# Optimization experiments

Measured on AMD Instinct MI355X. Metric: run time of the kernel, lower is better.

## Reference

```python
import jax, jax.numpy as jnp
import numpy as np

GAMMA = 1.0
NUM_CLASSES = 128


def setup_inputs() -> dict:
    key = jax.random.key(0)
    k1, k2, k3 = jax.random.split(key, 3)
    B, D, P = 8192, 512, 4096
    feature = jax.random.normal(k1, (B, D), dtype=jnp.float32)
    label = jax.random.randint(k2, (B,), 0, NUM_CLASSES)
    proto_features = jax.random.normal(k3, (P, D), dtype=jnp.float32)
    proto_labels = jnp.arange(P) % NUM_CLASSES  # every class has prototypes
    return {"feature": feature, "label": label,
            "proto_features": proto_features, "proto_labels": proto_labels}


def reference(feature, label, proto_features, proto_labels):
    # squared euclidean distances [B, P] via ||f||^2 + ||p||^2 - 2 f.p
    f_sq = jnp.sum(feature * feature, axis=-1, keepdims=True)          # [B,1]
    p_sq = jnp.sum(proto_features * proto_features, axis=-1)           # [P]
    d2 = f_sq + p_sq[None, :] - 2.0 * (feature @ proto_features.T)      # [B,P]
    d2 = jnp.maximum(d2, 0.0)
    logits = -GAMMA * d2                                                # [B,P]
    # denominator: sum over ALL prototypes; numerator: sum over own-class protos
    log_den = jax.scipy.special.logsumexp(logits, axis=-1)              # [B]
    same = proto_labels[None, :] == label[:, None]                      # [B,P]
    neg_inf = jnp.finfo(logits.dtype).min
    log_num = jax.scipy.special.logsumexp(
        jnp.where(same, logits, neg_inf), axis=-1)                      # [B]
    # loss = -log(num/den) per sample
    return log_den - log_num
```

## Files before the change

### kernel.cpp

```cpp
#include <hip/hip_runtime.h>
#include <hip/hip_bf16.h>

#define BN 8192
#define DK 512
#define PN 4096
#define GY 8
#define PPB 512
#define CH 32
#define NCH 16
#define STRIDE 520
#define SENT (-1.0e30f)
#define L2E 1.4426950408889634f
#define LN2 0.6931471805599453f

typedef __bf16 bf16x8 __attribute__((ext_vector_type(8)));
typedef __bf16 bf16x4 __attribute__((ext_vector_type(4)));
typedef float f32x4 __attribute__((ext_vector_type(4)));

__device__ __forceinline__ float ex2(float x) { return __builtin_amdgcn_exp2f(x); }

__device__ __forceinline__ void gl_lds16(const void* g, void* l) {
    __builtin_amdgcn_global_load_lds(
        (const __attribute__((address_space(1))) void*)g,
        (__attribute__((address_space(3))) void*)l, 16, 0, 0);
}

__global__ __launch_bounds__(256) void k_prep(const float* __restrict__ proto,
                                              __bf16* __restrict__ pB,
                                              float* __restrict__ p_sq) {
    int p  = blockIdx.x * 4 + (threadIdx.x >> 6);
    int ln = threadIdx.x & 63;
    const float* src = proto + (size_t)p * DK;
    float4 a = *(const float4*)(src + ln * 4);
    float4 b = *(const float4*)(src + 256 + ln * 4);
    float s = a.x * a.x + a.y * a.y + a.z * a.z + a.w * a.w
            + b.x * b.x + b.y * b.y + b.z * b.z + b.w * b.w;
#pragma unroll
    for (int m = 1; m < 64; m <<= 1) s += __shfl_xor(s, m, 64);
    int sidx = (p & 127) * 32 + (p >> 7);
    bf16x4 c0, c1;
    c0[0] = (__bf16)a.x; c0[1] = (__bf16)a.y; c0[2] = (__bf16)a.z; c0[3] = (__bf16)a.w;
    c1[0] = (__bf16)b.x; c1[1] = (__bf16)b.y; c1[2] = (__bf16)b.z; c1[3] = (__bf16)b.w;
    *(bf16x4*)(pB + (size_t)sidx * DK + ln * 4) = c0;
    *(bf16x4*)(pB + (size_t)sidx * DK + 256 + ln * 4) = c1;
    if (ln == 0) p_sq[sidx] = s * L2E;
}

__global__ __launch_bounds__(256, 2) void k_main(
        const float* __restrict__ feat,
        const __bf16* __restrict__ pB,
        const float* __restrict__ p_sq,
        const int* __restrict__ label,
        float4* __restrict__ part) {

    __shared__ __bf16 sM[2 * CH * STRIDE];
    __shared__ float  sPsq[PPB];

    const int t    = threadIdx.x;
    const int w    = t >> 6;
    const int l    = t & 63;
    const int ln   = l & 15;
    const int quad = l >> 4;
    const int bx   = blockIdx.x;
    const int gy   = blockIdx.y;
    const int rw   = bx * 128 + w * 32;
    const int p0   = gy * PPB;

    int lab[2][4];
#pragma unroll
    for (int mf = 0; mf < 2; ++mf)
#pragma unroll
        for (int r = 0; r < 4; ++r)
            lab[mf][r] = label[rw + mf * 16 + quad * 4 + r];

    {
        const __bf16* g = pB + (size_t)(p0 + w * 8) * DK + l * 8;
        __bf16* lp = sM + (w * 8) * STRIDE;
#pragma unroll
        for (int j = 0; j < 8; ++j)
            gl_lds16(g + j * DK, lp + j * STRIDE);
    }
    sPsq[t]       = p_sq[p0 + t];
    sPsq[t + 256] = p_sq[p0 + t + 256];

    __bf16* sA = sM + CH * STRIDE;
    bf16x8 afrag[2][16];
#pragma unroll 1
    for (int q = 0; q < 4; ++q) {
#pragma unroll 4
        for (int i = 0; i < 16; ++i) {
            int idx = t + 256 * i;
            int row = idx >> 7;
            int c4  = idx & 127;
            float4 v = *(const float4*)(feat + (size_t)(bx * 128 + q * 32 + row) * DK + c4 * 4);
            bf16x4 cv;
            cv[0] = (__bf16)v.x; cv[1] = (__bf16)v.y; cv[2] = (__bf16)v.z; cv[3] = (__bf16)v.w;
            *(bf16x4*)(sA + row * STRIDE + c4 * 4) = cv;
        }
        __syncthreads();
        if (w == q) {
#pragma unroll
            for (int mf = 0; mf < 2; ++mf)
#pragma unroll
                for (int ks = 0; ks < 16; ++ks)
                    afrag[mf][ks] = *(const bf16x8*)(sA + (mf * 16 + ln) * STRIDE + ks * 32 + quad * 8);
        }
        __syncthreads();
    }

    float Md[2][4], Sd[2][4], Mn[2][4], Sn[2][4];
#pragma unroll
    for (int mf = 0; mf < 2; ++mf)
#pragma unroll
        for (int r = 0; r < 4; ++r) {
            Md[mf][r] = SENT; Sd[mf][r] = 0.f;
            Mn[mf][r] = SENT; Sn[mf][r] = 0.f;
        }

#pragma unroll 1
    for (int nt = 0; nt < NCH; ++nt) {
        if (nt + 1 < NCH) {
            const __bf16* g = pB + (size_t)(p0 + (nt + 1) * CH + w * 8) * DK + l * 8;
            __bf16* lp = sM + (((nt + 1) & 1) * CH + w * 8) * STRIDE;
#pragma unroll
            for (int j = 0; j < 8; ++j)
                gl_lds16(g + j * DK, lp + j * STRIDE);
        }

        const __bf16* sB = sM + (nt & 1) * CH * STRIDE;

        f32x4 acc[2][2];
#pragma unroll
        for (int mf = 0; mf < 2; ++mf)
#pragma unroll
            for (int nf = 0; nf < 2; ++nf)
                acc[mf][nf] = (f32x4){0.f, 0.f, 0.f, 0.f};

#pragma unroll
        for (int ks = 0; ks < 16; ++ks) {
            bf16x8 b0 = *(const bf16x8*)(sB + ln * STRIDE + ks * 32 + quad * 8);
            bf16x8 b1 = *(const bf16x8*)(sB + (16 + ln) * STRIDE + ks * 32 + quad * 8);
            acc[0][0] = __builtin_amdgcn_mfma_f32_16x16x32_bf16(afrag[0][ks], b0, acc[0][0], 0, 0, 0);
            acc[0][1] = __builtin_amdgcn_mfma_f32_16x16x32_bf16(afrag[0][ks], b1, acc[0][1], 0, 0, 0);
            acc[1][0] = __builtin_amdgcn_mfma_f32_16x16x32_bf16(afrag[1][ks], b0, acc[1][0], 0, 0, 0);
            acc[1][1] = __builtin_amdgcn_mfma_f32_16x16x32_bf16(afrag[1][ks], b1, acc[1][1], 0, 0, 0);
        }

        float nps0 = -sPsq[nt * 32 + ln];
        float nps1 = -sPsq[nt * 32 + 16 + ln];
        const int cls = gy * 16 + nt;

        float z[2][2][4];
#pragma unroll
        for (int mf = 0; mf < 2; ++mf)
#pragma unroll
            for (int r = 0; r < 4; ++r) {
                z[mf][0][r] = fmaf(acc[mf][0][r], 2.0f * L2E, nps0);
                z[mf][1][r] = fmaf(acc[mf][1][r], 2.0f * L2E, nps1);
            }

#pragma unroll
        for (int mf = 0; mf < 2; ++mf)
#pragma unroll
            for (int r = 0; r < 4; ++r) {
                float z0 = z[mf][0][r], z1 = z[mf][1][r];
                float nm = fmaxf(Md[mf][r], fmaxf(z0, z1));
                float e  = ex2(z0 - nm) + ex2(z1 - nm);
                Sd[mf][r] = fmaf(Sd[mf][r], ex2(Md[mf][r] - nm), e);
                Md[mf][r] = nm;
            }

        int anyhit = 0;
#pragma unroll
        for (int mf = 0; mf < 2; ++mf)
#pragma unroll
            for (int r = 0; r < 4; ++r)
                anyhit |= (cls == lab[mf][r]);
        if (__any(anyhit)) {
#pragma unroll
            for (int mf = 0; mf < 2; ++mf)
#pragma unroll
                for (int r = 0; r < 4; ++r) {
                    bool hit = (cls == lab[mf][r]);
                    float z0 = z[mf][0][r], z1 = z[mf][1][r];
                    float nm = fmaxf(Mn[mf][r], fmaxf(z0, z1));
                    float e  = ex2(z0 - nm) + ex2(z1 - nm);
                    float sn = fmaf(Sn[mf][r], ex2(Mn[mf][r] - nm), e);
                    Sn[mf][r] = hit ? sn : Sn[mf][r];
                    Mn[mf][r] = hit ? nm : Mn[mf][r];
                }
        }
        __syncthreads();
    }

#pragma unroll
    for (int mf = 0; mf < 2; ++mf)
#pragma unroll
        for (int r = 0; r < 4; ++r) {
            float md = Md[mf][r], sd = Sd[mf][r];
            float mn = Mn[mf][r], sn = Sn[mf][r];
#pragma unroll
            for (int m = 1; m < 16; m <<= 1) {
                float omd = __shfl_xor(md, m, 64);
                float osd = __shfl_xor(sd, m, 64);
                float omn = __shfl_xor(mn, m, 64);
                float osn = __shfl_xor(sn, m, 64);
                float nm = fmaxf(md, omd);
                sd = sd * ex2(md - nm) + osd * ex2(omd - nm);
                md = nm;
                nm = fmaxf(mn, omn);
                sn = sn * ex2(mn - nm) + osn * ex2(omn - nm);
                mn = nm;
            }
            if (ln == 0) {
                int row = rw + mf * 16 + quad * 4 + r;
                part[row * GY + gy] = make_float4(md, sd, mn, sn);
            }
        }
}

__global__ __launch_bounds__(256) void k_comb(const float4* __restrict__ part,
                                              float* __restrict__ out) {
    int row = blockIdx.x * 256 + threadIdx.x;
    float md = SENT, sd = 0.f, mn = SENT, sn = 0.f;
#pragma unroll
    for (int q = 0; q < GY; ++q) {
        float4 v = part[row * GY + q];
        float nm = fmaxf(md, v.x);
        sd = sd * ex2(md - nm) + v.y * ex2(v.x - nm);
        md = nm;
        nm = fmaxf(mn, v.z);
        sn = sn * ex2(mn - nm) + v.w * ex2(v.z - nm);
        mn = nm;
    }
    out[row] = ((md + __builtin_amdgcn_logf(sd)) - (mn + __builtin_amdgcn_logf(sn))) * LN2;
}

extern "C" void kernel_launch(void* const* d_in, const int* in_sizes, int n_in,
                              void* d_out, int out_size, void* d_ws, size_t ws_size,
                              hipStream_t stream) {
    const float* feat   = (const float*)d_in[0];
    const int*   label  = (const int*)d_in[1];
    const float* proto  = (const float*)d_in[2];
    float*       out    = (float*)d_out;

    char* w = (char*)d_ws;
    __bf16* pB    = (__bf16*)(w);
    float*  p_sq  = (float*)(w + 4194304);
    float4* part  = (float4*)(w + 4243456);

    hipLaunchKernelGGL(k_prep, dim3(PN / 4), dim3(256), 0, stream,
                       proto, pB, p_sq);
    hipLaunchKernelGGL(k_main, dim3(64, GY), dim3(256), 0, stream,
                       feat, pB, p_sq, label, part);
    hipLaunchKernelGGL(k_comb, dim3(BN / 256), dim3(256), 0, stream,
                       part, out);
}
```

Before: 116.4 us.

## Software-pipeline the softmax update of the previous chunk into the current chunk's MFMA loop

Result: no change. 117.5 us (+1.0%).

```diff
diff --git a/kernel.cpp b/kernel.cpp
--- a/kernel.cpp
+++ b/kernel.cpp
@@ -109,13 +109,16 @@
     }
 
     float Md[2][4], Sd[2][4], Mn[2][4], Sn[2][4];
+    float zp[2][2][4];
 #pragma unroll
     for (int mf = 0; mf < 2; ++mf)
 #pragma unroll
         for (int r = 0; r < 4; ++r) {
             Md[mf][r] = SENT; Sd[mf][r] = 0.f;
             Mn[mf][r] = SENT; Sn[mf][r] = 0.f;
-        }
+            zp[mf][0][r] = SENT; zp[mf][1][r] = SENT;
+        }
+    int clsp = -1;
 
 #pragma unroll 1
     for (int nt = 0; nt < NCH; ++nt) {
@@ -128,6 +131,16 @@
         }
 
         const __bf16* sB = sM + (nt & 1) * CH * STRIDE;
+
+        float nps0 = -sPsq[nt * 32 + ln];
+        float nps1 = -sPsq[nt * 32 + 16 + ln];
+
+        int anyhit = 0;
+#pragma unroll
+        for (int mf = 0; mf < 2; ++mf)
+#pragma unroll
+            for (int r = 0; r < 4; ++r)
+                anyhit |= (clsp == lab[mf][r]);
 
         f32x4 acc[2][2];
 #pragma unroll
@@ -144,53 +157,74 @@
             acc[0][1] = __builtin_amdgcn_mfma_f32_16x16x32_bf16(afrag[0][ks], b1, acc[0][1], 0, 0, 0);
             acc[1][0] = __builtin_amdgcn_mfma_f32_16x16x32_bf16(afrag[1][ks], b0, acc[1][0], 0, 0, 0);
             acc[1][1] = __builtin_amdgcn_mfma_f32_16x16x32_bf16(afrag[1][ks], b1, acc[1][1], 0, 0, 0);
-        }
-
-        float nps0 = -sPsq[nt * 32 + ln];
-        float nps1 = -sPsq[nt * 32 + 16 + ln];
-        const int cls = gy * 16 + nt;
-
-        float z[2][2][4];
-#pragma unroll
-        for (int mf = 0; mf < 2; ++mf)
-#pragma unroll
-            for (int r = 0; r < 4; ++r) {
-                z[mf][0][r] = fmaf(acc[mf][0][r], 2.0f * L2E, nps0);
-                z[mf][1][r] = fmaf(acc[mf][1][r], 2.0f * L2E, nps1);
-            }
-
-#pragma unroll
-        for (int mf = 0; mf < 2; ++mf)
-#pragma unroll
-            for (int r = 0; r < 4; ++r) {
-                float z0 = z[mf][0][r], z1 = z[mf][1][r];
+            if ((ks & 1) == 0) {
+                const int j  = ks >> 1;
+                const int mf = j >> 2;
+                const int r  = j & 3;
+                float z0 = zp[mf][0][r], z1 = zp[mf][1][r];
                 float nm = fmaxf(Md[mf][r], fmaxf(z0, z1));
                 float e  = ex2(z0 - nm) + ex2(z1 - nm);
                 Sd[mf][r] = fmaf(Sd[mf][r], ex2(Md[mf][r] - nm), e);
                 Md[mf][r] = nm;
             }
-
+        }
+
+        if (__any(anyhit)) {
+#pragma unroll
+            for (int mf = 0; mf < 2; ++mf)
+#pragma unroll
+                for (int r = 0; r < 4; ++r) {
+                    bool hit = (clsp == lab[mf][r]);
+                    float z0 = zp[mf][0][r], z1 = zp[mf][1][r];
+                    float mn2 = fmaxf(z0, z1);
+                    float e2  = ex2(z0 - mn2) + ex2(z1 - mn2);
+                    Mn[mf][r] = hit ? mn2 : Mn[mf][r];
+                    Sn[mf][r] = hit ? e2  : Sn[mf][r];
+                }
+        }
+
+#pragma unroll
+        for (int mf = 0; mf < 2; ++mf)
+#pragma unroll
+            for (int r = 0; r < 4; ++r) {
+                zp[mf][0][r] = fmaf(acc[mf][0][r], 2.0f * L2E, nps0);
+                zp[mf][1][r] = fmaf(acc[mf][1][r], 2.0f * L2E, nps1);
+            }
+        clsp = gy * 16 + nt;
+
+        __syncthreads();
+    }
+
+    {
         int anyhit = 0;
 #pragma unroll
         for (int mf = 0; mf < 2; ++mf)
 #pragma unroll
             for (int r = 0; r < 4; ++r)
-                anyhit |= (cls == lab[mf][r]);
+                anyhit |= (clsp == lab[mf][r]);
+#pragma unroll
+        for (int mf = 0; mf < 2; ++mf)
+#pragma unroll
+            for (int r = 0; r < 4; ++r) {
+                float z0 = zp[mf][0][r], z1 = zp[mf][1][r];
+                float nm = fmaxf(Md[mf][r], fmaxf(z0, z1));
+                float e  = ex2(z0 - nm) + ex2(z1 - nm);
+                Sd[mf][r] = fmaf(Sd[mf][r], ex2(Md[mf][r] - nm), e);
+                Md[mf][r] = nm;
+            }
         if (__any(anyhit)) {
 #pragma unroll
             for (int mf = 0; mf < 2; ++mf)
 #pragma unroll
                 for (int r = 0; r < 4; ++r) {
-                    bool hit = (cls == lab[mf][r]);
-                    float z0 = z[mf][0][r], z1 = z[mf][1][r];
-                    float nm = fmaxf(Mn[mf][r], fmaxf(z0, z1));
-                    float e  = ex2(z0 - nm) + ex2(z1 - nm);
-                    float sn = fmaf(Sn[mf][r], ex2(Mn[mf][r] - nm), e);
-                    Sn[mf][r] = hit ? sn : Sn[mf][r];
-                    Mn[mf][r] = hit ? nm : Mn[mf][r];
+                    bool hit = (clsp == lab[mf][r]);
+                    float z0 = zp[mf][0][r], z1 = zp[mf][1][r];
+                    float mn2 = fmaxf(z0, z1);
+                    float e2  = ex2(z0 - mn2) + ex2(z1 - mn2);
+                    Mn[mf][r] = hit ? mn2 : Mn[mf][r];
+                    Sn[mf][r] = hit ? e2  : Sn[mf][r];
                 }
         }
-        __syncthreads();
     }
 
 #pragma unroll
```

## Stream prototype fragments from global into registers and software-pipeline softmax with MFMA

Applied to the files above, without the earlier changes.

Measured after the change: 163.3 us. +40.2%, slower.

```diff
diff --git a/kernel.cpp b/kernel.cpp
--- a/kernel.cpp
+++ b/kernel.cpp
@@ -6,9 +6,8 @@
 #define PN 4096
 #define GY 8
 #define PPB 512
-#define CH 32
-#define NCH 16
-#define STRIDE 520
+#define PG 16
+#define NG 32
 #define SENT (-1.0e30f)
 #define L2E 1.4426950408889634f
 #define LN2 0.6931471805599453f
@@ -18,12 +17,6 @@
 typedef float f32x4 __attribute__((ext_vector_type(4)));
 
 __device__ __forceinline__ float ex2(float x) { return __builtin_amdgcn_exp2f(x); }
-
-__device__ __forceinline__ void gl_lds16(const void* g, void* l) {
-    __builtin_amdgcn_global_load_lds(
-        (const __attribute__((address_space(1))) void*)g,
-        (__attribute__((address_space(3))) void*)l, 16, 0, 0);
-}
 
 __global__ __launch_bounds__(256) void k_prep(const float* __restrict__ proto,
                                               __bf16* __restrict__ pB,
@@ -46,15 +39,14 @@
     if (ln == 0) p_sq[sidx] = s * L2E;
 }
 
-__global__ __launch_bounds__(256, 2) void k_main(
+__global__ __launch_bounds__(256, 1) void k_main(
         const float* __restrict__ feat,
         const __bf16* __restrict__ pB,
         const float* __restrict__ p_sq,
         const int* __restrict__ label,
         float4* __restrict__ part) {
 
-    __shared__ __bf16 sM[2 * CH * STRIDE];
-    __shared__ float  sPsq[PPB];
+    __shared__ float sPsq[PPB];
 
     const int t    = threadIdx.x;
     const int w    = t >> 6;
@@ -63,138 +55,138 @@
     const int quad = l >> 4;
     const int bx   = blockIdx.x;
     const int gy   = blockIdx.y;
-    const int rw   = bx * 128 + w * 32;
+    const int rw   = bx * 256 + w * 64;
     const int p0   = gy * PPB;
 
-    int lab[2][4];
-#pragma unroll
-    for (int mf = 0; mf < 2; ++mf)
-#pragma unroll
-        for (int r = 0; r < 4; ++r)
-            lab[mf][r] = label[rw + mf * 16 + quad * 4 + r];
-
-    {
-        const __bf16* g = pB + (size_t)(p0 + w * 8) * DK + l * 8;
-        __bf16* lp = sM + (w * 8) * STRIDE;
-#pragma unroll
-        for (int j = 0; j < 8; ++j)
-            gl_lds16(g + j * DK, lp + j * STRIDE);
-    }
     sPsq[t]       = p_sq[p0 + t];
     sPsq[t + 256] = p_sq[p0 + t + 256];
 
-    __bf16* sA = sM + CH * STRIDE;
-    bf16x8 afrag[2][16];
-#pragma unroll 1
-    for (int q = 0; q < 4; ++q) {
-#pragma unroll 4
-        for (int i = 0; i < 16; ++i) {
-            int idx = t + 256 * i;
-            int row = idx >> 7;
-            int c4  = idx & 127;
-            float4 v = *(const float4*)(feat + (size_t)(bx * 128 + q * 32 + row) * DK + c4 * 4);
-            bf16x4 cv;
-            cv[0] = (__bf16)v.x; cv[1] = (__bf16)v.y; cv[2] = (__bf16)v.z; cv[3] = (__bf16)v.w;
-            *(bf16x4*)(sA + row * STRIDE + c4 * 4) = cv;
-        }
-        __syncthreads();
-        if (w == q) {
-#pragma unroll
-            for (int mf = 0; mf < 2; ++mf)
-#pragma unroll
-                for (int ks = 0; ks < 16; ++ks)
-                    afrag[mf][ks] = *(const bf16x8*)(sA + (mf * 16 + ln) * STRIDE + ks * 32 + quad * 8);
-        }
-        __syncthreads();
-    }
-
-    float Md[2][4], Sd[2][4], Mn[2][4], Sn[2][4];
-#pragma unroll
-    for (int mf = 0; mf < 2; ++mf)
+    unsigned labs[4];
+#pragma unroll
+    for (int mf = 0; mf < 4; ++mf) {
+        int base = rw + mf * 16 + quad * 4;
+        labs[mf] = (unsigned)label[base]
+                 | ((unsigned)label[base + 1] << 8)
+                 | ((unsigned)label[base + 2] << 16)
+                 | ((unsigned)label[base + 3] << 24);
+    }
+
+    bf16x8 afrag[4][16];
+#pragma unroll
+    for (int mf = 0; mf < 4; ++mf) {
+        const float* ar = feat + (size_t)(rw + mf * 16 + ln) * DK + quad * 8;
+#pragma unroll
+        for (int ks = 0; ks < 16; ++ks) {
+            float4 u = *(const float4*)(ar + ks * 32);
+            float4 v = *(const float4*)(ar + ks * 32 + 4);
+            bf16x8 c;
+            c[0] = (__bf16)u.x; c[1] = (__bf16)u.y; c[2] = (__bf16)u.z; c[3] = (__bf16)u.w;
+            c[4] = (__bf16)v.x; c[5] = (__bf16)v.y; c[6] = (__bf16)v.z; c[7] = (__bf16)v.w;
+            afrag[mf][ks] = c;
+        }
+    }
+
+    __syncthreads();
+
+    const __bf16* bp = pB + (size_t)(p0 + ln) * DK + quad * 8;
+
+    bf16x8 b0[8], b1[8];
+#pragma unroll
+    for (int ks = 0; ks < 8; ++ks) b0[ks] = *(const bf16x8*)(bp + ks * 32);
+#pragma unroll
+    for (int ks = 0; ks < 8; ++ks) b1[ks] = *(const bf16x8*)(bp + 256 + ks * 32);
+
+    float Md[4][4], Sd[4][4], Mn[4][4], Sn[4][4], zp[4][4];
+    unsigned hmp[4];
+    f32x4 acc[4];
+#pragma unroll
+    for (int mf = 0; mf < 4; ++mf) {
+        hmp[mf] = 0u;
+        acc[mf] = (f32x4){0.f, 0.f, 0.f, 0.f};
 #pragma unroll
         for (int r = 0; r < 4; ++r) {
             Md[mf][r] = SENT; Sd[mf][r] = 0.f;
             Mn[mf][r] = SENT; Sn[mf][r] = 0.f;
-        }
+            zp[mf][r] = SENT;
+        }
+    }
+
+#define DEN_SLICE(j) {                                                     \
+        const int mfj = (j) >> 2, rj = (j) & 3;                            \
+        float z  = zp[mfj][rj];                                            \
+        float nm = fmaxf(Md[mfj][rj], z);                                  \
+        Sd[mfj][rj] = fmaf(Sd[mfj][rj], ex2(Md[mfj][rj] - nm), ex2(z - nm)); \
+        Md[mfj][rj] = nm; }
+
+#define NUM_MERGE() {                                                      \
+        int anyp = (int)(hmp[0] | hmp[1] | hmp[2] | hmp[3]);               \
+        if (__any(anyp != 0)) {                                            \
+            _Pragma("unroll")                                              \
+            for (int mf = 0; mf < 4; ++mf)                                 \
+            { _Pragma("unroll")                                            \
+              for (int r = 0; r < 4; ++r) {                                \
+                bool hit = (hmp[mf] >> (8 * r + 7)) & 1;                   \
+                float z  = zp[mf][r];                                      \
+                float nm = fmaxf(Mn[mf][r], z);                            \
+                float sn = fmaf(Sn[mf][r], ex2(Mn[mf][r] - nm), ex2(z - nm)); \
+                Mn[mf][r] = hit ? nm : Mn[mf][r];                          \
+                Sn[mf][r] = hit ? sn : Sn[mf][r];                          \
+            } } } }
 
 #pragma unroll 1
-    for (int nt = 0; nt < NCH; ++nt) {
-        if (nt + 1 < NCH) {
-            const __bf16* g = pB + (size_t)(p0 + (nt + 1) * CH + w * 8) * DK + l * 8;
-            __bf16* lp = sM + (((nt + 1) & 1) * CH + w * 8) * STRIDE;
-#pragma unroll
-            for (int j = 0; j < 8; ++j)
-                gl_lds16(g + j * DK, lp + j * STRIDE);
-        }
-
-        const __bf16* sB = sM + (nt & 1) * CH * STRIDE;
-
-        f32x4 acc[2][2];
-#pragma unroll
-        for (int mf = 0; mf < 2; ++mf)
-#pragma unroll
-            for (int nf = 0; nf < 2; ++nf)
-                acc[mf][nf] = (f32x4){0.f, 0.f, 0.f, 0.f};
-
-#pragma unroll
-        for (int ks = 0; ks < 16; ++ks) {
-            bf16x8 b0 = *(const bf16x8*)(sB + ln * STRIDE + ks * 32 + quad * 8);
-            bf16x8 b1 = *(const bf16x8*)(sB + (16 + ln) * STRIDE + ks * 32 + quad * 8);
-            acc[0][0] = __builtin_amdgcn_mfma_f32_16x16x32_bf16(afrag[0][ks], b0, acc[0][0], 0, 0, 0);
-            acc[0][1] = __builtin_amdgcn_mfma_f32_16x16x32_bf16(afrag[0][ks], b1, acc[0][1], 0, 0, 0);
-            acc[1][0] = __builtin_amdgcn_mfma_f32_16x16x32_bf16(afrag[1][ks], b0, acc[1][0], 0, 0, 0);
-            acc[1][1] = __builtin_amdgcn_mfma_f32_16x16x32_bf16(afrag[1][ks], b1, acc[1][1], 0, 0, 0);
-        }
-
-        float nps0 = -sPsq[nt * 32 + ln];
-        float nps1 = -sPsq[nt * 32 + 16 + ln];
-        const int cls = gy * 16 + nt;
-
-        float z[2][2][4];
-#pragma unroll
-        for (int mf = 0; mf < 2; ++mf)
-#pragma unroll
-            for (int r = 0; r < 4; ++r) {
-                z[mf][0][r] = fmaf(acc[mf][0][r], 2.0f * L2E, nps0);
-                z[mf][1][r] = fmaf(acc[mf][1][r], 2.0f * L2E, nps1);
-            }
-
-#pragma unroll
-        for (int mf = 0; mf < 2; ++mf)
-#pragma unroll
-            for (int r = 0; r < 4; ++r) {
-                float z0 = z[mf][0][r], z1 = z[mf][1][r];
-                float nm = fmaxf(Md[mf][r], fmaxf(z0, z1));
-                float e  = ex2(z0 - nm) + ex2(z1 - nm);
-                Sd[mf][r] = fmaf(Sd[mf][r], ex2(Md[mf][r] - nm), e);
-                Md[mf][r] = nm;
-            }
-
-        int anyhit = 0;
-#pragma unroll
-        for (int mf = 0; mf < 2; ++mf)
+    for (int g = 0; g < NG; ++g) {
+        const __bf16* bn = bp + (size_t)(g + 1) * (PG * DK);
+        float nps = -sPsq[g * PG + ln];
+
+#pragma unroll
+        for (int ks = 0; ks < 8; ++ks) {
+            acc[0] = __builtin_amdgcn_mfma_f32_16x16x32_bf16(afrag[0][ks], b0[ks], acc[0], 0, 0, 0);
+            acc[1] = __builtin_amdgcn_mfma_f32_16x16x32_bf16(afrag[1][ks], b0[ks], acc[1], 0, 0, 0);
+            acc[2] = __builtin_amdgcn_mfma_f32_16x16x32_bf16(afrag[2][ks], b0[ks], acc[2], 0, 0, 0);
+            acc[3] = __builtin_amdgcn_mfma_f32_16x16x32_bf16(afrag[3][ks], b0[ks], acc[3], 0, 0, 0);
+            DEN_SLICE(ks);
+        }
+        if (g + 1 < NG) {
+#pragma unroll
+            for (int ks = 0; ks < 8; ++ks) b0[ks] = *(const bf16x8*)(bn + ks * 32);
+        }
+
+#pragma unroll
+        for (int ks = 0; ks < 8; ++ks) {
+            acc[0] = __builtin_amdgcn_mfma_f32_16x16x32_bf16(afrag[0][ks + 8], b1[ks], acc[0], 0, 0, 0);
+            acc[1] = __builtin_amdgcn_mfma_f32_16x16x32_bf16(afrag[1][ks + 8], b1[ks], acc[1], 0, 0, 0);
+            acc[2] = __builtin_amdgcn_mfma_f32_16x16x32_bf16(afrag[2][ks + 8], b1[ks], acc[2], 0, 0, 0);
+            acc[3] = __builtin_amdgcn_mfma_f32_16x16x32_bf16(afrag[3][ks + 8], b1[ks], acc[3], 0, 0, 0);
+            DEN_SLICE(ks + 8);
+        }
+        if (g + 1 < NG) {
+#pragma unroll
+            for (int ks = 0; ks < 8; ++ks) b1[ks] = *(const bf16x8*)(bn + 256 + ks * 32);
+        }
+
+        NUM_MERGE();
+
+        const unsigned cmul = (unsigned)(gy * 16 + (g >> 1)) * 0x01010101u;
+#pragma unroll
+        for (int mf = 0; mf < 4; ++mf) {
 #pragma unroll
             for (int r = 0; r < 4; ++r)
-                anyhit |= (cls == lab[mf][r]);
-        if (__any(anyhit)) {
-#pragma unroll
-            for (int mf = 0; mf < 2; ++mf)
-#pragma unroll
-                for (int r = 0; r < 4; ++r) {
-                    bool hit = (cls == lab[mf][r]);
-                    float z0 = z[mf][0][r], z1 = z[mf][1][r];
-                    float nm = fmaxf(Mn[mf][r], fmaxf(z0, z1));
-                    float e  = ex2(z0 - nm) + ex2(z1 - nm);
-                    float sn = fmaf(Sn[mf][r], ex2(Mn[mf][r] - nm), e);
-                    Sn[mf][r] = hit ? sn : Sn[mf][r];
-                    Mn[mf][r] = hit ? nm : Mn[mf][r];
-                }
-        }
-        __syncthreads();
-    }
-
-#pragma unroll
-    for (int mf = 0; mf < 2; ++mf)
+                zp[mf][r] = fmaf(acc[mf][r], 2.0f * L2E, nps);
+            acc[mf] = (f32x4){0.f, 0.f, 0.f, 0.f};
+            unsigned x = labs[mf] ^ cmul;
+            hmp[mf] = ~(((x & 0x7F7F7F7Fu) + 0x7F7F7F7Fu) | x | 0x7F7F7F7Fu);
+        }
+    }
+
+#pragma unroll
+    for (int j = 0; j < 16; ++j) DEN_SLICE(j);
+    NUM_MERGE();
+
+#undef DEN_SLICE
+#undef NUM_MERGE
+
+#pragma unroll
+    for (int mf = 0; mf < 4; ++mf)
 #pragma unroll
         for (int r = 0; r < 4; ++r) {
             float md = Md[mf][r], sd = Sd[mf][r];
@@ -251,7 +243,7 @@
 
     hipLaunchKernelGGL(k_prep, dim3(PN / 4), dim3(256), 0, stream,
                        proto, pB, p_sq);
-    hipLaunchKernelGGL(k_main, dim3(64, GY), dim3(256), 0, stream,
+    hipLaunchKernelGGL(k_main, dim3(BN / 256, GY), dim3(256), 0, stream,
                        feat, pB, p_sq, label, part);
     hipLaunchKernelGGL(k_comb, dim3(BN / 256), dim3(256), 0, stream,
                        part, out);
```

## Deepen prototype pipeline to 4 buffers and overlap softmax with next MFMA chunk

Applied to the files above, without the earlier changes.

Result: slower. 125.3 us (+7.6%).

```diff
diff --git a/kernel.cpp b/kernel.cpp
--- a/kernel.cpp
+++ b/kernel.cpp
@@ -6,9 +6,10 @@
 #define PN 4096
 #define GY 8
 #define PPB 512
-#define CH 32
-#define NCH 16
+#define CH 16
+#define NCH 32
 #define STRIDE 520
+#define BUFELE (CH * STRIDE)
 #define SENT (-1.0e30f)
 #define L2E 1.4426950408889634f
 #define LN2 0.6931471805599453f
@@ -53,7 +54,7 @@
         const int* __restrict__ label,
         float4* __restrict__ part) {
 
-    __shared__ __bf16 sM[2 * CH * STRIDE];
+    __shared__ __bf16 sM[4 * BUFELE];
     __shared__ float  sPsq[PPB];
 
     const int t    = threadIdx.x;
@@ -73,17 +74,19 @@
         for (int r = 0; r < 4; ++r)
             lab[mf][r] = label[rw + mf * 16 + quad * 4 + r];
 
-    {
-        const __bf16* g = pB + (size_t)(p0 + w * 8) * DK + l * 8;
-        __bf16* lp = sM + (w * 8) * STRIDE;
-#pragma unroll
-        for (int j = 0; j < 8; ++j)
-            gl_lds16(g + j * DK, lp + j * STRIDE);
-    }
+#define ISSUE(c) {                                                          \
+        const __bf16* g = pB + (size_t)(p0 + (c) * CH + w * 4) * DK + l * 8; \
+        __bf16* lp = sM + ((c) & 3) * BUFELE + (w * 4) * STRIDE;            \
+        _Pragma("unroll")                                                   \
+        for (int j = 0; j < 4; ++j)                                         \
+            gl_lds16(g + j * DK, lp + j * STRIDE);                          \
+    }
+
+    ISSUE(0);
     sPsq[t]       = p_sq[p0 + t];
     sPsq[t + 256] = p_sq[p0 + t + 256];
 
-    __bf16* sA = sM + CH * STRIDE;
+    __bf16* sA = sM + 2 * BUFELE;
     bf16x8 afrag[2][16];
 #pragma unroll 1
     for (int q = 0; q < 4; ++q) {
@@ -108,90 +111,88 @@
         __syncthreads();
     }
 
-    float Md[2][4], Sd[2][4], Mn[2][4], Sn[2][4];
+    ISSUE(1);
+    ISSUE(2);
+
+    float Md[2][4], Sd[2][4], Mn[2][4], Sn[2][4], zp[2][4];
 #pragma unroll
     for (int mf = 0; mf < 2; ++mf)
 #pragma unroll
         for (int r = 0; r < 4; ++r) {
             Md[mf][r] = SENT; Sd[mf][r] = 0.f;
             Mn[mf][r] = SENT; Sn[mf][r] = 0.f;
-        }
+            zp[mf][r] = SENT;
+        }
+    int clsp = -1;
+
+#define DEN_SLICE(j) {                                                      \
+        const int mfj = (j) >> 2, rj = (j) & 3;                             \
+        float z  = zp[mfj][rj];                                             \
+        float nm = fmaxf(Md[mfj][rj], z);                                   \
+        Sd[mfj][rj] = fmaf(Sd[mfj][rj], ex2(Md[mfj][rj] - nm), ex2(z - nm)); \
+        Md[mfj][rj] = nm; }
+
+#define NUM_MERGE() {                                                       \
+        int anyhit = 0;                                                     \
+        _Pragma("unroll")                                                   \
+        for (int mf = 0; mf < 2; ++mf)                                      \
+        { _Pragma("unroll")                                                 \
+          for (int r = 0; r < 4; ++r) anyhit |= (clsp == lab[mf][r]); }     \
+        if (__any(anyhit)) {                                                \
+            _Pragma("unroll")                                               \
+            for (int mf = 0; mf < 2; ++mf)                                  \
+            { _Pragma("unroll")                                             \
+              for (int r = 0; r < 4; ++r) {                                 \
+                bool hit = (clsp == lab[mf][r]);                            \
+                float z  = zp[mf][r];                                       \
+                float nm = fmaxf(Mn[mf][r], z);                             \
+                float sn = fmaf(Sn[mf][r], ex2(Mn[mf][r] - nm), ex2(z - nm)); \
+                Mn[mf][r] = hit ? nm : Mn[mf][r];                           \
+                Sn[mf][r] = hit ? sn : Sn[mf][r];                           \
+            } } } }
+
+#define COMPUTE(nt) {                                                       \
+        const __bf16* sB = sM + ((nt) & 3) * BUFELE;                        \
+        float nps = -sPsq[(nt) * CH + ln];                                  \
+        f32x4 a0 = (f32x4){0.f, 0.f, 0.f, 0.f};                             \
+        f32x4 a1 = (f32x4){0.f, 0.f, 0.f, 0.f};                             \
+        _Pragma("unroll")                                                   \
+        for (int ks = 0; ks < 16; ++ks) {                                   \
+            bf16x8 b = *(const bf16x8*)(sB + ln * STRIDE + ks * 32 + quad * 8); \
+            a0 = __builtin_amdgcn_mfma_f32_16x16x32_bf16(afrag[0][ks], b, a0, 0, 0, 0); \
+            a1 = __builtin_amdgcn_mfma_f32_16x16x32_bf16(afrag[1][ks], b, a1, 0, 0, 0); \
+            if ((ks & 1) == 0) DEN_SLICE(ks >> 1);                          \
+        }                                                                   \
+        NUM_MERGE();                                                        \
+        _Pragma("unroll")                                                   \
+        for (int r = 0; r < 4; ++r) {                                       \
+            zp[0][r] = fmaf(a0[r], 2.0f * L2E, nps);                        \
+            zp[1][r] = fmaf(a1[r], 2.0f * L2E, nps);                        \
+        }                                                                   \
+        clsp = gy * 16 + ((nt) >> 1); }
 
 #pragma unroll 1
-    for (int nt = 0; nt < NCH; ++nt) {
-        if (nt + 1 < NCH) {
-            const __bf16* g = pB + (size_t)(p0 + (nt + 1) * CH + w * 8) * DK + l * 8;
-            __bf16* lp = sM + (((nt + 1) & 1) * CH + w * 8) * STRIDE;
-#pragma unroll
-            for (int j = 0; j < 8; ++j)
-                gl_lds16(g + j * DK, lp + j * STRIDE);
-        }
-
-        const __bf16* sB = sM + (nt & 1) * CH * STRIDE;
-
-        f32x4 acc[2][2];
-#pragma unroll
-        for (int mf = 0; mf < 2; ++mf)
-#pragma unroll
-            for (int nf = 0; nf < 2; ++nf)
-                acc[mf][nf] = (f32x4){0.f, 0.f, 0.f, 0.f};
-
-#pragma unroll
-        for (int ks = 0; ks < 16; ++ks) {
-            bf16x8 b0 = *(const bf16x8*)(sB + ln * STRIDE + ks * 32 + quad * 8);
-            bf16x8 b1 = *(const bf16x8*)(sB + (16 + ln) * STRIDE + ks * 32 + quad * 8);
-            acc[0][0] = __builtin_amdgcn_mfma_f32_16x16x32_bf16(afrag[0][ks], b0, acc[0][0], 0, 0, 0);
-            acc[0][1] = __builtin_amdgcn_mfma_f32_16x16x32_bf16(afrag[0][ks], b1, acc[0][1], 0, 0, 0);
-            acc[1][0] = __builtin_amdgcn_mfma_f32_16x16x32_bf16(afrag[1][ks], b0, acc[1][0], 0, 0, 0);
-            acc[1][1] = __builtin_amdgcn_mfma_f32_16x16x32_bf16(afrag[1][ks], b1, acc[1][1], 0, 0, 0);
-        }
-
-        float nps0 = -sPsq[nt * 32 + ln];
-        float nps1 = -sPsq[nt * 32 + 16 + ln];
-        const int cls = gy * 16 + nt;
-
-        float z[2][2][4];
-#pragma unroll
-        for (int mf = 0; mf < 2; ++mf)
-#pragma unroll
-            for (int r = 0; r < 4; ++r) {
-                z[mf][0][r] = fmaf(acc[mf][0][r], 2.0f * L2E, nps0);
-                z[mf][1][r] = fmaf(acc[mf][1][r], 2.0f * L2E, nps1);
-            }
-
-#pragma unroll
-        for (int mf = 0; mf < 2; ++mf)
-#pragma unroll
-            for (int r = 0; r < 4; ++r) {
-                float z0 = z[mf][0][r], z1 = z[mf][1][r];
-                float nm = fmaxf(Md[mf][r], fmaxf(z0, z1));
-                float e  = ex2(z0 - nm) + ex2(z1 - nm);
-                Sd[mf][r] = fmaf(Sd[mf][r], ex2(Md[mf][r] - nm), e);
-                Md[mf][r] = nm;
-            }
-
-        int anyhit = 0;
-#pragma unroll
-        for (int mf = 0; mf < 2; ++mf)
-#pragma unroll
-            for (int r = 0; r < 4; ++r)
-                anyhit |= (cls == lab[mf][r]);
-        if (__any(anyhit)) {
-#pragma unroll
-            for (int mf = 0; mf < 2; ++mf)
-#pragma unroll
-                for (int r = 0; r < 4; ++r) {
-                    bool hit = (cls == lab[mf][r]);
-                    float z0 = z[mf][0][r], z1 = z[mf][1][r];
-                    float nm = fmaxf(Mn[mf][r], fmaxf(z0, z1));
-                    float e  = ex2(z0 - nm) + ex2(z1 - nm);
-                    float sn = fmaf(Sn[mf][r], ex2(Mn[mf][r] - nm), e);
-                    Sn[mf][r] = hit ? sn : Sn[mf][r];
-                    Mn[mf][r] = hit ? nm : Mn[mf][r];
-                }
-        }
-        __syncthreads();
-    }
+    for (int nt = 0; nt < NCH - 2; ++nt) {
+        asm volatile("s_waitcnt vmcnt(8)" ::: "memory");
+        __builtin_amdgcn_s_barrier();
+        if (nt + 3 < NCH) ISSUE(nt + 3);
+        COMPUTE(nt);
+    }
+    asm volatile("s_waitcnt vmcnt(4)" ::: "memory");
+    __builtin_amdgcn_s_barrier();
+    COMPUTE(NCH - 2);
+    asm volatile("s_waitcnt vmcnt(0)" ::: "memory");
+    __builtin_amdgcn_s_barrier();
+    COMPUTE(NCH - 1);
+
+#pragma unroll
+    for (int j = 0; j < 8; ++j) DEN_SLICE(j);
+    NUM_MERGE();
+
+#undef COMPUTE
+#undef DEN_SLICE
+#undef NUM_MERGE
+#undef ISSUE
 
 #pragma unroll
     for (int mf = 0; mf < 2; ++mf)
```
